# Optimization experiments

Measured on AMD Instinct MI355X. Metric: run time of the kernel, lower is better.

Reference implementation:

```python
import jax, jax.numpy as jnp
import numpy as np

EMBED = 1024
HEADS = 16
HDIM = EMBED // HEADS
MASK_OUT = -10000.0


def setup_inputs() -> dict:
    key = jax.random.key(0)
    ks = jax.random.split(key, 12)
    B, S = 4, 1023
    scale = 0.02
    return {
        "word_hidden_states": jax.random.normal(ks[0], (B, S, EMBED), jnp.float32),
        "image_hidden_states": jax.random.normal(ks[1], (B, EMBED), jnp.float32),
        "attention_mask": jnp.zeros((B, 1, 1, S), jnp.float32),
        "c_attn_w": jax.random.normal(ks[2], (EMBED, 3 * EMBED), jnp.float32) * scale,
        "c_attn_b": jnp.zeros((3 * EMBED,), jnp.float32),
        "c_proj_w": jax.random.normal(ks[3], (EMBED, EMBED), jnp.float32) * scale,
        "c_proj_b": jnp.zeros((EMBED,), jnp.float32),
        "uk_w": jax.random.normal(ks[4], (EMBED, EMBED), jnp.float32) * scale,
        "uk_b": jnp.zeros((EMBED,), jnp.float32),
        "uv_w": jax.random.normal(ks[5], (EMBED, EMBED), jnp.float32) * scale,
        "uv_b": jnp.zeros((EMBED,), jnp.float32),
    }


def _split_heads(t):
    # [B, T, E] -> [B, H, T, D]
    B, T, _ = t.shape
    return t.reshape(B, T, HEADS, HDIM).transpose(0, 2, 1, 3)


def reference(word_hidden_states, image_hidden_states, attention_mask,
              c_attn_w, c_attn_b, c_proj_w, c_proj_b,
              uk_w, uk_b, uv_w, uv_b):
    B, S, _ = word_hidden_states.shape
    # c_attn: Conv1D -> x @ W + b, then split into q, k, v
    qkv = word_hidden_states @ c_attn_w + c_attn_b          # [B, S, 3E]
    q_word, k_word, v_word = jnp.split(qkv, 3, axis=-1)
    # image key/value via nn.Linear (x @ W^T + b)
    img = image_hidden_states[:, None, :]                    # [B, 1, E]
    k_img = img @ uk_w.T + uk_b
    v_img = img @ uv_w.T + uv_b
    k = jnp.concatenate([k_img, k_word], axis=1)             # [B, S+1, E]
    v = jnp.concatenate([v_img, v_word], axis=1)

    q = _split_heads(q_word)                                 # [B, H, S, D]
    k = _split_heads(k)                                      # [B, H, S+1, D]
    v = _split_heads(v)

    scores = jnp.einsum("bhqd,bhkd->bhqk", q, k) / jnp.sqrt(jnp.float32(HDIM))
    # causal mask: tril rows [1 : S+1], cols [: S+1] of max_positions grid
    # -> query i may attend key j iff j <= i + 1 (image token always visible)
    qi = jnp.arange(S)[:, None]
    kj = jnp.arange(S + 1)[None, :]
    causal = kj <= qi + 1                                     # [S, S+1]
    scores = jnp.where(causal[None, None], scores, jnp.float32(MASK_OUT))
    # prepend zero column to additive attention mask for the image token
    zero_col = jnp.zeros(attention_mask.shape[:-1] + (1,), attention_mask.dtype)
    mask = jnp.concatenate([zero_col, attention_mask], axis=-1)  # [B,1,1,S+1]
    scores = scores + mask
    attn = jax.nn.softmax(scores, axis=-1)                    # dropout: eval mode (identity)
    out = jnp.einsum("bhqk,bhkd->bhqd", attn, v)              # [B, H, S, D]
    out = out.transpose(0, 2, 1, 3).reshape(B, S, EMBED)      # merge heads
    out = out @ c_proj_w + c_proj_b                           # c_proj Conv1D
    return out
```

## Files before the change

### kernel.cpp

```cpp
#include <hip/hip_runtime.h>

#define EMBED 1024
#define HEADS 16
#define HDIM 64
#define SQ 1023
#define SK 1024
#define MTOK 4092
#define MPAD 4096

typedef __attribute__((ext_vector_type(8))) short short8;
typedef __attribute__((ext_vector_type(4))) float floatx4;

static __device__ __forceinline__ unsigned short f2bf(float f) {
  union { float f; unsigned u; } v; v.f = f;
  unsigned u = v.u;
  u += 0x7fffu + ((u >> 16) & 1u);
  return (unsigned short)(u >> 16);
}

static __device__ __forceinline__ void gld16(const unsigned short* g, unsigned short* l) {
  typedef const __attribute__((address_space(1))) unsigned int guint;
  typedef __attribute__((address_space(3))) unsigned int luint;
  __builtin_amdgcn_global_load_lds((guint*)(const void*)g, (luint*)(void*)l, 16, 0, 0);
}


__global__ __launch_bounds__(256) void k_cast_word(const float* __restrict__ W,
                                                   unsigned short* __restrict__ A) {
  int idx = (blockIdx.x * 256 + threadIdx.x) * 8;
  int row = idx >> 10;
  short8 v;
  if (row < MTOK) {
    const float4* p = (const float4*)(W + idx);
    float4 a = p[0], b = p[1];
    v[0] = (short)f2bf(a.x); v[1] = (short)f2bf(a.y);
    v[2] = (short)f2bf(a.z); v[3] = (short)f2bf(a.w);
    v[4] = (short)f2bf(b.x); v[5] = (short)f2bf(b.y);
    v[6] = (short)f2bf(b.z); v[7] = (short)f2bf(b.w);
  } else {
#pragma unroll
    for (int i = 0; i < 8; i++) v[i] = 0;
  }
  *(short8*)(A + idx) = v;
}

__global__ __launch_bounds__(256) void k_transpose_cast(const float* __restrict__ W,
                                                        unsigned short* __restrict__ Wt,
                                                        int K, int N) {
  __shared__ float T[32][33];
  int tx = threadIdx.x & 31, ty = threadIdx.x >> 5;
  int n0 = blockIdx.x * 32, k0 = blockIdx.y * 32;
#pragma unroll
  for (int i = 0; i < 4; i++) {
    int r = ty + i * 8;
    T[r][tx] = W[(k0 + r) * N + n0 + tx];
  }
  __syncthreads();
#pragma unroll
  for (int i = 0; i < 4; i++) {
    int r = ty + i * 8;
    Wt[(n0 + r) * K + k0 + tx] = f2bf(T[tx][r]);
  }
}

__global__ __launch_bounds__(256) void k_img_kv(const float* __restrict__ img,
    const float* __restrict__ ukw, const float* __restrict__ ukb,
    const float* __restrict__ uvw, const float* __restrict__ uvb,
    unsigned short* __restrict__ Kb, unsigned short* __restrict__ Vb) {
  int wid = blockIdx.x * 4 + (threadIdx.x >> 6);
  int lane = threadIdx.x & 63;
  int which = wid >> 12;
  int bb = (wid >> 10) & 3;
  int n = wid & 1023;
  const float* W = which ? uvw : ukw;
  const float* bias = which ? uvb : ukb;
  unsigned short* out = which ? Vb : Kb;
  const float* x = img + bb * 1024;
  const float* w = W + n * 1024;
  float s = 0.f;
#pragma unroll
  for (int i = 0; i < 16; i++) { int k = i * 64 + lane; s += x[k] * w[k]; }
#pragma unroll
  for (int off = 32; off; off >>= 1) s += __shfl_xor(s, off);
  if (lane == 0) {
    int h = n >> 6, d = n & 63;
    out[((bb * HEADS + h) * SK + 0) * HDIM + d] = f2bf(s + bias[n]);
  }
}

__global__ void k_zero_qpad(unsigned short* __restrict__ Qb) {
  int i = blockIdx.x * 256 + threadIdx.x;
  int bh = i >> 6, d = i & 63;
  Qb[(bh * SK + (SK - 1)) * HDIM + d] = 0;
}

__global__ __launch_bounds__(256) void k_vt(const unsigned short* __restrict__ V,
                                            unsigned short* __restrict__ Vt) {
  __shared__ unsigned short T[64 * 72];
  int t = threadIdx.x;
  int sb = blockIdx.x, bh = blockIdx.y;
  const unsigned short* src = V + (bh * SK + sb * 64) * HDIM;
#pragma unroll
  for (int i = 0; i < 2; i++) {
    int r = i * 32 + (t >> 3), c8 = t & 7;
    short8 v = *(const short8*)(src + r * 64 + c8 * 8);
    *(short8*)(T + r * 72 + c8 * 8) = v;
  }
  __syncthreads();
#pragma unroll
  for (int i = 0; i < 2; i++) {
    int cid = i * 256 + t;
    int d = cid >> 3, s8 = cid & 7;
    short8 v;
#pragma unroll
    for (int e = 0; e < 8; e++) v[e] = (short)T[(s8 * 8 + e) * 72 + d];
    *(short8*)(Vt + (bh * 64 + d) * SK + sb * 64 + s8 * 8) = v;
  }
}

template <int EPI>
__global__ __launch_bounds__(256, 2) void k_gemm(
    const unsigned short* __restrict__ A, const unsigned short* __restrict__ Bt,
    int Kdim, const float* __restrict__ bias,
    unsigned short* __restrict__ Qb, unsigned short* __restrict__ Kb,
    unsigned short* __restrict__ Vb, float* __restrict__ out) {
  __shared__ __attribute__((aligned(16))) unsigned short Sm[16384];
  unsigned short* As = Sm;
  unsigned short* Bs = Sm + 8192;
  int t = threadIdx.x, lane = t & 63, w = t >> 6;
  int quad = lane >> 4, l16 = lane & 15;
  int m0 = blockIdx.y * 128, n0 = blockIdx.x * 128;
  int waveM = (w >> 1) * 64, waveN = (w & 1) * 64;
  int rs = t >> 3, cs = t & 7;

  floatx4 acc[4][4];
#pragma unroll
  for (int i = 0; i < 4; i++)
#pragma unroll
    for (int j = 0; j < 4; j++)
#pragma unroll
      for (int e = 0; e < 4; e++) acc[i][j][e] = 0.f;

  const unsigned short* Ag = A + m0 * Kdim;
  const unsigned short* Bg = Bt + n0 * Kdim;

  for (int k0 = 0; k0 < Kdim; k0 += 64) {
    __syncthreads();
#pragma unroll
    for (int i = 0; i < 4; i++) {
      int r = i * 32 + rs;
      gld16(Ag + r * Kdim + k0 + ((cs ^ (r & 7)) * 8), As + i * 2048 + t * 8);
    }
#pragma unroll
    for (int i = 0; i < 4; i++) {
      int r = i * 32 + rs;
      gld16(Bg + r * Kdim + k0 + ((cs ^ (r & 7)) * 8), Bs + i * 2048 + t * 8);
    }
    __syncthreads();
    short8 af[2][4], bf8[2][4];
#pragma unroll
    for (int kk = 0; kk < 2; kk++) {
#pragma unroll
      for (int mr = 0; mr < 4; mr++) {
        int row = waveM + mr * 16 + l16;
        af[kk][mr] = *(const short8*)(As + row * 64 + (((kk * 4 + quad) ^ (row & 7)) * 8));
      }
#pragma unroll
      for (int nc = 0; nc < 4; nc++) {
        int row = waveN + nc * 16 + l16;
        bf8[kk][nc] = *(const short8*)(Bs + row * 64 + (((kk * 4 + quad) ^ (row & 7)) * 8));
      }
    }
#pragma unroll
    for (int kk = 0; kk < 2; kk++)
#pragma unroll
      for (int mr = 0; mr < 4; mr++)
#pragma unroll
        for (int nc = 0; nc < 4; nc++)
          acc[mr][nc] = __builtin_amdgcn_mfma_f32_16x16x32_bf16(af[kk][mr], bf8[kk][nc], acc[mr][nc], 0, 0, 0);
  }

  float bv[4];
#pragma unroll
  for (int nc = 0; nc < 4; nc++) bv[nc] = bias[n0 + waveN + nc * 16 + l16];

  if (EPI == 0) {
    unsigned short* Cs = Sm;
    for (int p = 0; p < 2; p++) {
      __syncthreads();
      if ((w >> 1) == p) {
#pragma unroll
        for (int mr = 0; mr < 4; mr++)
#pragma unroll
          for (int nc = 0; nc < 4; nc++)
#pragma unroll
            for (int r = 0; r < 4; r++) {
              int lrow = mr * 16 + quad * 4 + r;
              int lcol = waveN + nc * 16 + l16;
              Cs[lrow * 128 + (((lcol >> 3) ^ (lrow & 7)) * 8) + (lcol & 7)] =
                  f2bf(acc[mr][nc][r] + bv[nc]);
            }
      }
      __syncthreads();
#pragma unroll
      for (int i = 0; i < 4; i++) {
        int cid = i * 256 + t;
        int lr = cid >> 4, c8 = cid & 15;
        short8 v = *(const short8*)(Cs + lr * 128 + ((c8 ^ (lr & 7)) * 8));
        int gm = m0 + p * 64 + lr;
        if (gm < MTOK) {
          int gn = n0 + c8 * 8;
          int which = gn >> 10, e = gn & 1023;
          int h = e >> 6, d0 = e & 63;
          unsigned short* dst = (which == 0) ? Qb : (which == 1) ? Kb : Vb;
          int sofs = (which == 0) ? 0 : 1;
          int bb = (unsigned)gm / 1023u;
          int s = gm - bb * 1023;
          *(short8*)(dst + ((bb * HEADS + h) * SK + s + sofs) * HDIM + d0) = v;
        }
      }
    }
  } else {
#pragma unroll
    for (int nc = 0; nc < 4; nc++) {
      int gn = n0 + waveN + nc * 16 + l16;
#pragma unroll
      for (int mr = 0; mr < 4; mr++) {
#pragma unroll
        for (int r = 0; r < 4; r++) {
          int gm = m0 + waveM + mr * 16 + quad * 4 + r;
          if (gm < MTOK) out[gm * EMBED + gn] = acc[mr][nc][r] + bv[nc];
        }
      }
    }
  }
}

__global__ __launch_bounds__(256, 2) void k_flash(
    const unsigned short* __restrict__ Qb, const unsigned short* __restrict__ Kb,
    const unsigned short* __restrict__ Vtg, const float* __restrict__ am,
    unsigned short* __restrict__ Ao) {
  __shared__ __attribute__((aligned(16))) unsigned short Qs[4096];
  __shared__ __attribute__((aligned(16))) unsigned short Ks[8192];
  __shared__ __attribute__((aligned(16))) unsigned short Vs[8192];
  __shared__ __attribute__((aligned(16))) unsigned short Ps[4 * 2304];

  int t = threadIdx.x, lane = t & 63, w = t >> 6;
  int quad = lane >> 4, l16 = lane & 15;
  int tq = blockIdx.x, bh = blockIdx.y;
  int bb = bh >> 4, h = bh & 15;

#pragma unroll
  for (int i = 0; i < 2; i++) {
    int r = i * 32 + (t >> 3), gc = (t & 7) ^ (r & 7);
    gld16(Qb + (bh * SK + tq * 64 + r) * HDIM + gc * 8, Qs + i * 2048 + t * 8);
  }

  float m_i[4], l_i[4];
  floatx4 acc_o[4];
#pragma unroll
  for (int r = 0; r < 4; r++) { m_i[r] = -1e30f; l_i[r] = 0.f; }
#pragma unroll
  for (int n = 0; n < 4; n++)
#pragma unroll
    for (int e = 0; e < 4; e++) acc_o[n][e] = 0.f;

  unsigned short* Pw = Ps + w * 2304;
  int jmax = min((tq + 1) >> 1, 7);
  for (int j = 0; j <= jmax; j++) {
    __syncthreads();
#pragma unroll
    for (int i = 0; i < 4; i++) {
      int r = i * 32 + (t >> 3), gc = (t & 7) ^ (r & 7);
      gld16(Kb + (bh * SK + j * 128 + r) * HDIM + gc * 8, Ks + i * 2048 + t * 8);
    }
#pragma unroll
    for (int i = 0; i < 4; i++) {
      int d = i * 16 + (t >> 4), gc = (t & 15) ^ (d & 7);
      gld16(Vtg + (bh * 64 + d) * SK + j * 128 + gc * 8, Vs + i * 2048 + t * 8);
    }
    __syncthreads();

    floatx4 sacc[8];
#pragma unroll
    for (int n = 0; n < 8; n++)
#pragma unroll
      for (int e = 0; e < 4; e++) sacc[n][e] = 0.f;
#pragma unroll
    for (int kk = 0; kk < 2; kk++) {
      int qrow = w * 16 + l16;
      short8 a = *(const short8*)(Qs + qrow * 64 + (((kk * 4 + quad) ^ (qrow & 7)) * 8));
#pragma unroll
      for (int nc = 0; nc < 8; nc++) {
        int krow = nc * 16 + l16;
        short8 b = *(const short8*)(Ks + krow * 64 + (((kk * 4 + quad) ^ (krow & 7)) * 8));
        sacc[nc] = __builtin_amdgcn_mfma_f32_16x16x32_bf16(a, b, sacc[nc], 0, 0, 0);
      }
    }

    bool needmask = (j * 128 + 127 > tq * 64 + 1);
    int qbase = tq * 64 + w * 16 + quad * 4;
    float sval[8][4], tmax[4];
#pragma unroll
    for (int r = 0; r < 4; r++) tmax[r] = -1e30f;
#pragma unroll
    for (int nc = 0; nc < 8; nc++) {
      int kg = j * 128 + nc * 16 + l16;
      float amv = (kg >= 1) ? am[bb * SQ + kg - 1] : 0.f;
#pragma unroll
      for (int r = 0; r < 4; r++) {
        float sc = sacc[nc][r] * 0.125f;
        if (needmask && kg > qbase + r + 1) sc = -10000.0f;
        sc += amv;
        sval[nc][r] = sc;
        tmax[r] = fmaxf(tmax[r], sc);
      }
    }
#pragma unroll
    for (int off = 1; off < 16; off <<= 1)
#pragma unroll
      for (int r = 0; r < 4; r++) tmax[r] = fmaxf(tmax[r], __shfl_xor(tmax[r], off));

    float alpha[4];
#pragma unroll
    for (int r = 0; r < 4; r++) {
      float mn = fmaxf(m_i[r], tmax[r]);
      alpha[r] = __expf(m_i[r] - mn);
      m_i[r] = mn;
    }
    float rsum[4] = {0.f, 0.f, 0.f, 0.f};
#pragma unroll
    for (int nc = 0; nc < 8; nc++)
#pragma unroll
      for (int r = 0; r < 4; r++) {
        float p = __expf(sval[nc][r] - m_i[r]);
        sval[nc][r] = p;
        rsum[r] += p;
      }
#pragma unroll
    for (int off = 1; off < 16; off <<= 1)
#pragma unroll
      for (int r = 0; r < 4; r++) rsum[r] += __shfl_xor(rsum[r], off);
#pragma unroll
    for (int r = 0; r < 4; r++) l_i[r] = l_i[r] * alpha[r] + rsum[r];
#pragma unroll
    for (int n = 0; n < 4; n++)
#pragma unroll
      for (int e = 0; e < 4; e++) acc_o[n][e] *= alpha[e];

#pragma unroll
    for (int nc = 0; nc < 8; nc++)
#pragma unroll
      for (int r = 0; r < 4; r++)
        Pw[(quad * 4 + r) * 144 + nc * 16 + l16] = f2bf(sval[nc][r]);

#pragma unroll
    for (int kk2 = 0; kk2 < 4; kk2++) {
      short8 a = *(const short8*)(Pw + l16 * 144 + (kk2 * 4 + quad) * 8);
#pragma unroll
      for (int n = 0; n < 4; n++) {
        int vrow = n * 16 + l16;
        short8 b = *(const short8*)(Vs + vrow * 128 + (((kk2 * 4 + quad) ^ (vrow & 7)) * 8));
        acc_o[n] = __builtin_amdgcn_mfma_f32_16x16x32_bf16(a, b, acc_o[n], 0, 0, 0);
      }
    }
  }

  float inv[4];
#pragma unroll
  for (int r = 0; r < 4; r++) inv[r] = 1.f / l_i[r];
  unsigned short* Os = Ps;
  __syncthreads();
#pragma unroll
  for (int n = 0; n < 4; n++)
#pragma unroll
    for (int r = 0; r < 4; r++)
      Os[(w * 16 + quad * 4 + r) * 72 + n * 16 + l16] = f2bf(acc_o[n][r] * inv[r]);
  __syncthreads();
#pragma unroll
  for (int i = 0; i < 2; i++) {
    int cid = i * 256 + t, r = cid >> 3, c8 = cid & 7;
    int q = tq * 64 + r;
    if (q < SQ)
      *(short8*)(Ao + (bb * SQ + q) * EMBED + h * HDIM + c8 * 8) =
          *(const short8*)(Os + r * 72 + c8 * 8);
  }
}

extern "C" void kernel_launch(void* const* d_in, const int* in_sizes, int n_in,
                              void* d_out, int out_size, void* d_ws, size_t ws_size,
                              hipStream_t stream) {
  const float* word   = (const float*)d_in[0];
  const float* img    = (const float*)d_in[1];
  const float* amask  = (const float*)d_in[2];
  const float* attn_w = (const float*)d_in[3];
  const float* attn_b = (const float*)d_in[4];
  const float* proj_w = (const float*)d_in[5];
  const float* proj_b = (const float*)d_in[6];
  const float* ukw    = (const float*)d_in[7];
  const float* ukb    = (const float*)d_in[8];
  const float* uvw    = (const float*)d_in[9];
  const float* uvb    = (const float*)d_in[10];
  float* out = (float*)d_out;

  char* ws = (char*)d_ws;
  unsigned short* Aw     = (unsigned short*)(ws);
  unsigned short* WtAttn = (unsigned short*)(ws + 8388608);
  unsigned short* WtProj = (unsigned short*)(ws + 14680064);
  unsigned short* Vtg    = (unsigned short*)(ws + 8388608);
  unsigned short* Qb     = (unsigned short*)(ws + 16777216);
  unsigned short* Kb     = (unsigned short*)(ws + 25165824);
  unsigned short* Vb     = (unsigned short*)(ws + 33554432);
  unsigned short* Ao     = Aw;

  k_cast_word<<<2048, 256, 0, stream>>>(word, Aw);
  k_transpose_cast<<<dim3(96, 32), 256, 0, stream>>>(attn_w, WtAttn, 1024, 3072);
  k_img_kv<<<2048, 256, 0, stream>>>(img, ukw, ukb, uvw, uvb, Kb, Vb);
  k_zero_qpad<<<16, 256, 0, stream>>>(Qb);
  k_gemm<0><<<dim3(24, 32), 256, 0, stream>>>(Aw, WtAttn, 1024, attn_b, Qb, Kb, Vb, nullptr);
  k_vt<<<dim3(16, 64), 256, 0, stream>>>(Vb, Vtg);
  k_flash<<<dim3(16, 64), 256, 0, stream>>>(Qb, Kb, Vtg, amask, Ao);
  k_transpose_cast<<<dim3(32, 32), 256, 0, stream>>>(proj_w, WtProj, 1024, 1024);
  k_gemm<1><<<dim3(8, 32), 256, 0, stream>>>(Ao, WtProj, 1024, proj_b, nullptr, nullptr, nullptr, out);
}
```

Measured before the change: 240.0 us.

## Merge prep kernels, write V transposed from QKV GEMM, trim flash attention work

Folds the word cast, both weight transposes, the image K/V projection and the Q padding zeroing into one launch. The QKV GEMM epilogue now writes V directly in transposed layout, which removes the separate transpose kernel. The flash kernel keeps Q in registers and uses exp2 with a pre-scaled log2e factor. It skips waves and column chunks that are fully causally masked, schedules the heaviest query tiles first, raises occupancy to 3 blocks, and uses truncating bf16 conversion for P. Costs: scalar strided stores for the V transpose, a small rounding change in P, and higher register pressure.

```diff
diff --git a/kernel.cpp b/kernel.cpp
--- a/kernel.cpp
+++ b/kernel.cpp
@@ -24,97 +24,78 @@
   __builtin_amdgcn_global_load_lds((guint*)(const void*)g, (luint*)(void*)l, 16, 0, 0);
 }
 
-
-__global__ __launch_bounds__(256) void k_cast_word(const float* __restrict__ W,
-                                                   unsigned short* __restrict__ A) {
-  int idx = (blockIdx.x * 256 + threadIdx.x) * 8;
-  int row = idx >> 10;
-  short8 v;
-  if (row < MTOK) {
-    const float4* p = (const float4*)(W + idx);
-    float4 a = p[0], b = p[1];
-    v[0] = (short)f2bf(a.x); v[1] = (short)f2bf(a.y);
-    v[2] = (short)f2bf(a.z); v[3] = (short)f2bf(a.w);
-    v[4] = (short)f2bf(b.x); v[5] = (short)f2bf(b.y);
-    v[6] = (short)f2bf(b.z); v[7] = (short)f2bf(b.w);
-  } else {
-#pragma unroll
-    for (int i = 0; i < 8; i++) v[i] = 0;
-  }
-  *(short8*)(A + idx) = v;
-}
-
-__global__ __launch_bounds__(256) void k_transpose_cast(const float* __restrict__ W,
-                                                        unsigned short* __restrict__ Wt,
-                                                        int K, int N) {
-  __shared__ float T[32][33];
-  int tx = threadIdx.x & 31, ty = threadIdx.x >> 5;
-  int n0 = blockIdx.x * 32, k0 = blockIdx.y * 32;
-#pragma unroll
-  for (int i = 0; i < 4; i++) {
-    int r = ty + i * 8;
-    T[r][tx] = W[(k0 + r) * N + n0 + tx];
-  }
-  __syncthreads();
-#pragma unroll
-  for (int i = 0; i < 4; i++) {
-    int r = ty + i * 8;
-    Wt[(n0 + r) * K + k0 + tx] = f2bf(T[tx][r]);
-  }
-}
-
-__global__ __launch_bounds__(256) void k_img_kv(const float* __restrict__ img,
+__global__ __launch_bounds__(256) void k_prep(
+    const float* __restrict__ word, const float* __restrict__ attn_w,
+    const float* __restrict__ proj_w, const float* __restrict__ img,
     const float* __restrict__ ukw, const float* __restrict__ ukb,
     const float* __restrict__ uvw, const float* __restrict__ uvb,
-    unsigned short* __restrict__ Kb, unsigned short* __restrict__ Vb) {
-  int wid = blockIdx.x * 4 + (threadIdx.x >> 6);
-  int lane = threadIdx.x & 63;
-  int which = wid >> 12;
-  int bb = (wid >> 10) & 3;
-  int n = wid & 1023;
-  const float* W = which ? uvw : ukw;
-  const float* bias = which ? uvb : ukb;
-  unsigned short* out = which ? Vb : Kb;
-  const float* x = img + bb * 1024;
-  const float* w = W + n * 1024;
-  float s = 0.f;
-#pragma unroll
-  for (int i = 0; i < 16; i++) { int k = i * 64 + lane; s += x[k] * w[k]; }
-#pragma unroll
-  for (int off = 32; off; off >>= 1) s += __shfl_xor(s, off);
-  if (lane == 0) {
-    int h = n >> 6, d = n & 63;
-    out[((bb * HEADS + h) * SK + 0) * HDIM + d] = f2bf(s + bias[n]);
-  }
-}
-
-__global__ void k_zero_qpad(unsigned short* __restrict__ Qb) {
-  int i = blockIdx.x * 256 + threadIdx.x;
-  int bh = i >> 6, d = i & 63;
-  Qb[(bh * SK + (SK - 1)) * HDIM + d] = 0;
-}
-
-__global__ __launch_bounds__(256) void k_vt(const unsigned short* __restrict__ V,
-                                            unsigned short* __restrict__ Vt) {
-  __shared__ unsigned short T[64 * 72];
-  int t = threadIdx.x;
-  int sb = blockIdx.x, bh = blockIdx.y;
-  const unsigned short* src = V + (bh * SK + sb * 64) * HDIM;
-#pragma unroll
-  for (int i = 0; i < 2; i++) {
-    int r = i * 32 + (t >> 3), c8 = t & 7;
-    short8 v = *(const short8*)(src + r * 64 + c8 * 8);
-    *(short8*)(T + r * 72 + c8 * 8) = v;
-  }
-  __syncthreads();
-#pragma unroll
-  for (int i = 0; i < 2; i++) {
-    int cid = i * 256 + t;
-    int d = cid >> 3, s8 = cid & 7;
+    unsigned short* __restrict__ A, unsigned short* __restrict__ WtA,
+    unsigned short* __restrict__ WtP, unsigned short* __restrict__ Qb,
+    unsigned short* __restrict__ Kb, unsigned short* __restrict__ Vt) {
+  __shared__ float T[32][33];
+  int bx = blockIdx.x, t = threadIdx.x;
+  if (bx < 2048) {
+    int idx = (bx * 256 + t) * 8;
+    int row = idx >> 10;
     short8 v;
-#pragma unroll
-    for (int e = 0; e < 8; e++) v[e] = (short)T[(s8 * 8 + e) * 72 + d];
-    *(short8*)(Vt + (bh * 64 + d) * SK + sb * 64 + s8 * 8) = v;
+    if (row < MTOK) {
+      const float4* p = (const float4*)(word + idx);
+      float4 a = p[0], b = p[1];
+      v[0] = (short)f2bf(a.x); v[1] = (short)f2bf(a.y);
+      v[2] = (short)f2bf(a.z); v[3] = (short)f2bf(a.w);
+      v[4] = (short)f2bf(b.x); v[5] = (short)f2bf(b.y);
+      v[6] = (short)f2bf(b.z); v[7] = (short)f2bf(b.w);
+    } else {
+#pragma unroll
+      for (int i = 0; i < 8; i++) v[i] = 0;
+    }
+    *(short8*)(A + idx) = v;
+  } else if (bx < 6144) {
+    const float* W; unsigned short* Wt; int N, n0, k0;
+    if (bx < 5120) {
+      int r = bx - 2048; W = attn_w; Wt = WtA; N = 3072;
+      n0 = (r % 96) * 32; k0 = (r / 96) * 32;
+    } else {
+      int r = bx - 5120; W = proj_w; Wt = WtP; N = 1024;
+      n0 = (r & 31) * 32; k0 = (r >> 5) * 32;
+    }
+    int tx = t & 31, ty = t >> 5;
+#pragma unroll
+    for (int i = 0; i < 4; i++) {
+      int r = ty + i * 8;
+      T[r][tx] = W[(k0 + r) * N + n0 + tx];
+    }
+    __syncthreads();
+#pragma unroll
+    for (int i = 0; i < 4; i++) {
+      int r = ty + i * 8;
+      Wt[(n0 + r) * 1024 + k0 + tx] = f2bf(T[tx][r]);
+    }
+  } else if (bx < 8192) {
+    int wid = (bx - 6144) * 4 + (t >> 6);
+    int lane = t & 63;
+    int which = wid >> 12;
+    int bb = (wid >> 10) & 3;
+    int n = wid & 1023;
+    const float* W = which ? uvw : ukw;
+    const float* bias = which ? uvb : ukb;
+    const float* x = img + bb * 1024;
+    const float* w = W + n * 1024;
+    float s = 0.f;
+#pragma unroll
+    for (int i = 0; i < 16; i++) { int k = i * 64 + lane; s += x[k] * w[k]; }
+#pragma unroll
+    for (int off = 32; off; off >>= 1) s += __shfl_xor(s, off);
+    if (lane == 0) {
+      int h = n >> 6, d = n & 63;
+      unsigned short val = f2bf(s + bias[n]);
+      if (which == 0) Kb[((bb * HEADS + h) * SK + 0) * HDIM + d] = val;
+      else            Vt[((bb * HEADS + h) * HDIM + d) * SK + 0] = val;
+    }
+  } else {
+    int i = (bx - 8192) * 256 + t;
+    int bh = i >> 6, d = i & 63;
+    Qb[(bh * SK + (SK - 1)) * HDIM + d] = 0;
   }
 }
 
@@ -123,7 +104,7 @@
     const unsigned short* __restrict__ A, const unsigned short* __restrict__ Bt,
     int Kdim, const float* __restrict__ bias,
     unsigned short* __restrict__ Qb, unsigned short* __restrict__ Kb,
-    unsigned short* __restrict__ Vb, float* __restrict__ out) {
+    unsigned short* __restrict__ VtOut, float* __restrict__ out) {
   __shared__ __attribute__((aligned(16))) unsigned short Sm[16384];
   unsigned short* As = Sm;
   unsigned short* Bs = Sm + 8192;
@@ -186,6 +167,7 @@
 
   if (EPI == 0) {
     unsigned short* Cs = Sm;
+    int which0 = n0 >> 10;
     for (int p = 0; p < 2; p++) {
       __syncthreads();
       if ((w >> 1) == p) {
@@ -197,26 +179,43 @@
             for (int r = 0; r < 4; r++) {
               int lrow = mr * 16 + quad * 4 + r;
               int lcol = waveN + nc * 16 + l16;
-              Cs[lrow * 128 + (((lcol >> 3) ^ (lrow & 7)) * 8) + (lcol & 7)] =
+              Cs[lrow * 128 + ((((lcol >> 3) + lrow) & 15) * 8) + (lcol & 7)] =
                   f2bf(acc[mr][nc][r] + bv[nc]);
             }
       }
       __syncthreads();
-#pragma unroll
-      for (int i = 0; i < 4; i++) {
-        int cid = i * 256 + t;
-        int lr = cid >> 4, c8 = cid & 15;
-        short8 v = *(const short8*)(Cs + lr * 128 + ((c8 ^ (lr & 7)) * 8));
-        int gm = m0 + p * 64 + lr;
-        if (gm < MTOK) {
-          int gn = n0 + c8 * 8;
-          int which = gn >> 10, e = gn & 1023;
+      if (which0 == 2) {
+        int tok = t & 63;
+        int gm = m0 + p * 64 + tok;
+        int cb = (t >> 6) * 32;
+        bool okm = (gm < MTOK);
+        int bb = (unsigned)gm / 1023u;
+        int s = gm - bb * 1023;
+#pragma unroll
+        for (int it = 0; it < 32; it++) {
+          int c = cb + it;
+          unsigned short val = Cs[tok * 128 + ((((c >> 3) + tok) & 15) * 8) + (c & 7)];
+          int e = (n0 + c) & 1023;
           int h = e >> 6, d0 = e & 63;
-          unsigned short* dst = (which == 0) ? Qb : (which == 1) ? Kb : Vb;
-          int sofs = (which == 0) ? 0 : 1;
-          int bb = (unsigned)gm / 1023u;
-          int s = gm - bb * 1023;
-          *(short8*)(dst + ((bb * HEADS + h) * SK + s + sofs) * HDIM + d0) = v;
+          if (okm) VtOut[((bb * HEADS + h) * HDIM + d0) * SK + s + 1] = val;
+        }
+      } else {
+        unsigned short* dst = which0 ? Kb : Qb;
+        int sofs = which0;
+#pragma unroll
+        for (int i = 0; i < 4; i++) {
+          int cid = i * 256 + t;
+          int lr = cid >> 4, c8 = cid & 15;
+          short8 v = *(const short8*)(Cs + lr * 128 + (((c8 + lr) & 15) * 8));
+          int gm = m0 + p * 64 + lr;
+          if (gm < MTOK) {
+            int gn = n0 + c8 * 8;
+            int e = gn & 1023;
+            int h = e >> 6, d0 = e & 63;
+            int bb = (unsigned)gm / 1023u;
+            int s = gm - bb * 1023;
+            *(short8*)(dst + ((bb * HEADS + h) * SK + s + sofs) * HDIM + d0) = v;
+          }
         }
       }
     }
@@ -236,25 +235,31 @@
   }
 }
 
-__global__ __launch_bounds__(256, 2) void k_flash(
+__global__ __launch_bounds__(256, 3) void k_flash(
     const unsigned short* __restrict__ Qb, const unsigned short* __restrict__ Kb,
     const unsigned short* __restrict__ Vtg, const float* __restrict__ am,
     unsigned short* __restrict__ Ao) {
-  __shared__ __attribute__((aligned(16))) unsigned short Qs[4096];
   __shared__ __attribute__((aligned(16))) unsigned short Ks[8192];
   __shared__ __attribute__((aligned(16))) unsigned short Vs[8192];
-  __shared__ __attribute__((aligned(16))) unsigned short Ps[4 * 2304];
+  __shared__ __attribute__((aligned(16))) unsigned short Ps[8192];
 
   int t = threadIdx.x, lane = t & 63, w = t >> 6;
   int quad = lane >> 4, l16 = lane & 15;
-  int tq = blockIdx.x, bh = blockIdx.y;
+  int tq = 15 - (int)blockIdx.x;
+  int bh = blockIdx.y;
   int bb = bh >> 4, h = bh & 15;
 
-#pragma unroll
-  for (int i = 0; i < 2; i++) {
-    int r = i * 32 + (t >> 3), gc = (t & 7) ^ (r & 7);
-    gld16(Qb + (bh * SK + tq * 64 + r) * HDIM + gc * 8, Qs + i * 2048 + t * 8);
-  }
+  short8 qf[2];
+  {
+    int qrow = tq * 64 + w * 16 + l16;
+#pragma unroll
+    for (int kk = 0; kk < 2; kk++)
+      qf[kk] = *(const short8*)(Qb + (bh * SK + qrow) * HDIM + (kk * 4 + quad) * 8);
+  }
+
+  const float SCL = 0.18033688011f;
+  const float MASKV = -14426.950408f;
+  const float L2E = 1.44269504089f;
 
   float m_i[4], l_i[4];
   floatx4 acc_o[4];
@@ -265,7 +270,7 @@
 #pragma unroll
     for (int e = 0; e < 4; e++) acc_o[n][e] = 0.f;
 
-  unsigned short* Pw = Ps + w * 2304;
+  unsigned short* Pw = Ps + w * 2048;
   int jmax = min((tq + 1) >> 1, 7);
   for (int j = 0; j <= jmax; j++) {
     __syncthreads();
@@ -277,91 +282,105 @@
 #pragma unroll
     for (int i = 0; i < 4; i++) {
       int d = i * 16 + (t >> 4), gc = (t & 15) ^ (d & 7);
-      gld16(Vtg + (bh * 64 + d) * SK + j * 128 + gc * 8, Vs + i * 2048 + t * 8);
+      gld16(Vtg + (bh * HDIM + d) * SK + j * 128 + gc * 8, Vs + i * 2048 + t * 8);
     }
     __syncthreads();
 
-    floatx4 sacc[8];
-#pragma unroll
-    for (int n = 0; n < 8; n++)
-#pragma unroll
-      for (int e = 0; e < 4; e++) sacc[n][e] = 0.f;
-#pragma unroll
-    for (int kk = 0; kk < 2; kk++) {
-      int qrow = w * 16 + l16;
-      short8 a = *(const short8*)(Qs + qrow * 64 + (((kk * 4 + quad) ^ (qrow & 7)) * 8));
+    bool active_w = (j * 128 <= tq * 64 + w * 16 + 16);
+    if (active_w) {
+      floatx4 sacc[8];
+#pragma unroll
+      for (int n = 0; n < 8; n++)
+#pragma unroll
+        for (int e = 0; e < 4; e++) sacc[n][e] = 0.f;
+#pragma unroll
+      for (int kk = 0; kk < 2; kk++) {
+#pragma unroll
+        for (int nc = 0; nc < 8; nc++) {
+          int krow = nc * 16 + l16;
+          short8 b = *(const short8*)(Ks + krow * 64 + (((kk * 4 + quad) ^ (krow & 7)) * 8));
+          sacc[nc] = __builtin_amdgcn_mfma_f32_16x16x32_bf16(qf[kk], b, sacc[nc], 0, 0, 0);
+        }
+      }
+
+      int qbase = tq * 64 + w * 16 + quad * 4;
+      float sval[8][4], tmax[4];
+      bool deadnc[8];
+#pragma unroll
+      for (int r = 0; r < 4; r++) tmax[r] = -1e30f;
 #pragma unroll
       for (int nc = 0; nc < 8; nc++) {
-        int krow = nc * 16 + l16;
-        short8 b = *(const short8*)(Ks + krow * 64 + (((kk * 4 + quad) ^ (krow & 7)) * 8));
-        sacc[nc] = __builtin_amdgcn_mfma_f32_16x16x32_bf16(a, b, sacc[nc], 0, 0, 0);
-      }
-    }
-
-    bool needmask = (j * 128 + 127 > tq * 64 + 1);
-    int qbase = tq * 64 + w * 16 + quad * 4;
-    float sval[8][4], tmax[4];
-#pragma unroll
-    for (int r = 0; r < 4; r++) tmax[r] = -1e30f;
-#pragma unroll
-    for (int nc = 0; nc < 8; nc++) {
-      int kg = j * 128 + nc * 16 + l16;
-      float amv = (kg >= 1) ? am[bb * SQ + kg - 1] : 0.f;
+        deadnc[nc] = (j * 128 + nc * 16) > (tq * 64 + w * 16 + 16);
+        if (deadnc[nc]) {
+#pragma unroll
+          for (int r = 0; r < 4; r++) sval[nc][r] = 0.f;
+        } else {
+          int kg = j * 128 + nc * 16 + l16;
+          float amv = ((kg >= 1) ? am[bb * SQ + kg - 1] : 0.f) * L2E;
+#pragma unroll
+          for (int r = 0; r < 4; r++) {
+            float sc = sacc[nc][r] * SCL;
+            if (kg > qbase + r + 1) sc = MASKV;
+            sc += amv;
+            sval[nc][r] = sc;
+            tmax[r] = fmaxf(tmax[r], sc);
+          }
+        }
+      }
+#pragma unroll
+      for (int off = 1; off < 16; off <<= 1)
+#pragma unroll
+        for (int r = 0; r < 4; r++) tmax[r] = fmaxf(tmax[r], __shfl_xor(tmax[r], off));
+
+      float alpha[4];
 #pragma unroll
       for (int r = 0; r < 4; r++) {
-        float sc = sacc[nc][r] * 0.125f;
-        if (needmask && kg > qbase + r + 1) sc = -10000.0f;
-        sc += amv;
-        sval[nc][r] = sc;
-        tmax[r] = fmaxf(tmax[r], sc);
-      }
-    }
-#pragma unroll
-    for (int off = 1; off < 16; off <<= 1)
-#pragma unroll
-      for (int r = 0; r < 4; r++) tmax[r] = fmaxf(tmax[r], __shfl_xor(tmax[r], off));
-
-    float alpha[4];
-#pragma unroll
-    for (int r = 0; r < 4; r++) {
-      float mn = fmaxf(m_i[r], tmax[r]);
-      alpha[r] = __expf(m_i[r] - mn);
-      m_i[r] = mn;
-    }
-    float rsum[4] = {0.f, 0.f, 0.f, 0.f};
-#pragma unroll
-    for (int nc = 0; nc < 8; nc++)
-#pragma unroll
-      for (int r = 0; r < 4; r++) {
-        float p = __expf(sval[nc][r] - m_i[r]);
-        sval[nc][r] = p;
-        rsum[r] += p;
-      }
-#pragma unroll
-    for (int off = 1; off < 16; off <<= 1)
-#pragma unroll
-      for (int r = 0; r < 4; r++) rsum[r] += __shfl_xor(rsum[r], off);
-#pragma unroll
-    for (int r = 0; r < 4; r++) l_i[r] = l_i[r] * alpha[r] + rsum[r];
-#pragma unroll
-    for (int n = 0; n < 4; n++)
-#pragma unroll
-      for (int e = 0; e < 4; e++) acc_o[n][e] *= alpha[e];
-
-#pragma unroll
-    for (int nc = 0; nc < 8; nc++)
-#pragma unroll
-      for (int r = 0; r < 4; r++)
-        Pw[(quad * 4 + r) * 144 + nc * 16 + l16] = f2bf(sval[nc][r]);
-
-#pragma unroll
-    for (int kk2 = 0; kk2 < 4; kk2++) {
-      short8 a = *(const short8*)(Pw + l16 * 144 + (kk2 * 4 + quad) * 8);
-#pragma unroll
-      for (int n = 0; n < 4; n++) {
-        int vrow = n * 16 + l16;
-        short8 b = *(const short8*)(Vs + vrow * 128 + (((kk2 * 4 + quad) ^ (vrow & 7)) * 8));
-        acc_o[n] = __builtin_amdgcn_mfma_f32_16x16x32_bf16(a, b, acc_o[n], 0, 0, 0);
+        float mn = fmaxf(m_i[r], tmax[r]);
+        alpha[r] = __builtin_amdgcn_exp2f(m_i[r] - mn);
+        m_i[r] = mn;
+      }
+      float rsum[4] = {0.f, 0.f, 0.f, 0.f};
+#pragma unroll
+      for (int nc = 0; nc < 8; nc++) {
+        if (!deadnc[nc]) {
+#pragma unroll
+          for (int r = 0; r < 4; r++) {
+            float p = __builtin_amdgcn_exp2f(sval[nc][r] - m_i[r]);
+            sval[nc][r] = p;
+            rsum[r] += p;
+          }
+        }
+      }
+#pragma unroll
+      for (int off = 1; off < 16; off <<= 1)
+#pragma unroll
+        for (int r = 0; r < 4; r++) rsum[r] += __shfl_xor(rsum[r], off);
+#pragma unroll
+      for (int r = 0; r < 4; r++) l_i[r] = l_i[r] * alpha[r] + rsum[r];
+#pragma unroll
+      for (int n = 0; n < 4; n++)
+#pragma unroll
+        for (int e = 0; e < 4; e++) acc_o[n][e] *= alpha[e];
+
+#pragma unroll
+      for (int nc = 0; nc < 8; nc++)
+#pragma unroll
+        for (int r = 0; r < 4; r++) {
+          int row = quad * 4 + r;
+          union { float f; unsigned u; } cv; cv.f = sval[nc][r];
+          Pw[row * 128 + (((nc * 2 + (l16 >> 3)) ^ (row & 7)) * 8) + (l16 & 7)] =
+              (unsigned short)(cv.u >> 16);
+        }
+
+#pragma unroll
+      for (int kk2 = 0; kk2 < 4; kk2++) {
+        short8 a = *(const short8*)(Pw + l16 * 128 + (((kk2 * 4 + quad) ^ (l16 & 7)) * 8));
+#pragma unroll
+        for (int n = 0; n < 4; n++) {
+          int vrow = n * 16 + l16;
+          short8 b = *(const short8*)(Vs + vrow * 128 + (((kk2 * 4 + quad) ^ (vrow & 7)) * 8));
+          acc_o[n] = __builtin_amdgcn_mfma_f32_16x16x32_bf16(a, b, acc_o[n], 0, 0, 0);
+        }
       }
     }
   }
@@ -374,16 +393,19 @@
 #pragma unroll
   for (int n = 0; n < 4; n++)
 #pragma unroll
-    for (int r = 0; r < 4; r++)
-      Os[(w * 16 + quad * 4 + r) * 72 + n * 16 + l16] = f2bf(acc_o[n][r] * inv[r]);
+    for (int r = 0; r < 4; r++) {
+      int row = w * 16 + quad * 4 + r, col = n * 16 + l16;
+      Os[row * 64 + ((((col >> 3) + row) & 7) * 8) + (col & 7)] = f2bf(acc_o[n][r] * inv[r]);
+    }
   __syncthreads();
 #pragma unroll
   for (int i = 0; i < 2; i++) {
     int cid = i * 256 + t, r = cid >> 3, c8 = cid & 7;
     int q = tq * 64 + r;
-    if (q < SQ)
-      *(short8*)(Ao + (bb * SQ + q) * EMBED + h * HDIM + c8 * 8) =
-          *(const short8*)(Os + r * 72 + c8 * 8);
+    if (q < SQ) {
+      short8 v = *(const short8*)(Os + r * 64 + (((c8 + r) & 7) * 8));
+      *(short8*)(Ao + (bb * SQ + q) * EMBED + h * HDIM + c8 * 8) = v;
+    }
   }
 }
 
@@ -407,19 +429,14 @@
   unsigned short* Aw     = (unsigned short*)(ws);
   unsigned short* WtAttn = (unsigned short*)(ws + 8388608);
   unsigned short* WtProj = (unsigned short*)(ws + 14680064);
-  unsigned short* Vtg    = (unsigned short*)(ws + 8388608);
   unsigned short* Qb     = (unsigned short*)(ws + 16777216);
   unsigned short* Kb     = (unsigned short*)(ws + 25165824);
-  unsigned short* Vb     = (unsigned short*)(ws + 33554432);
+  unsigned short* Vtg    = (unsigned short*)(ws + 33554432);
   unsigned short* Ao     = Aw;
 
-  k_cast_word<<<2048, 256, 0, stream>>>(word, Aw);
-  k_transpose_cast<<<dim3(96, 32), 256, 0, stream>>>(attn_w, WtAttn, 1024, 3072);
-  k_img_kv<<<2048, 256, 0, stream>>>(img, ukw, ukb, uvw, uvb, Kb, Vb);
-  k_zero_qpad<<<16, 256, 0, stream>>>(Qb);
-  k_gemm<0><<<dim3(24, 32), 256, 0, stream>>>(Aw, WtAttn, 1024, attn_b, Qb, Kb, Vb, nullptr);
-  k_vt<<<dim3(16, 64), 256, 0, stream>>>(Vb, Vtg);
+  k_prep<<<8208, 256, 0, stream>>>(word, attn_w, proj_w, img, ukw, ukb, uvw, uvb,
+                                   Aw, WtAttn, WtProj, Qb, Kb, Vtg);
+  k_gemm<0><<<dim3(24, 32), 256, 0, stream>>>(Aw, WtAttn, 1024, attn_b, Qb, Kb, Vtg, nullptr);
   k_flash<<<dim3(16, 64), 256, 0, stream>>>(Qb, Kb, Vtg, amask, Ao);
-  k_transpose_cast<<<dim3(32, 32), 256, 0, stream>>>(proj_w, WtProj, 1024, 1024);
   k_gemm<1><<<dim3(8, 32), 256, 0, stream>>>(Ao, WtProj, 1024, proj_b, nullptr, nullptr, nullptr, out);
 }
```

After: 240.4 us. Within noise of the previous version (+0.2%).
